# Kernel optimization log

Hardware: AMD Instinct MI355X
Metric: run time of the kernel (lower is better)

## Reference

```python
import jax, jax.numpy as jnp
import numpy as np

B, S, D_IN, D_OUT, HID, E, SHARE, TOPK = 4, 2048, 1024, 1024, 2048, 8, 1, 2


def setup_inputs() -> dict:
    key = jax.random.key(0)
    ks = jax.random.split(key, 12)
    s_in = 1.0 / np.sqrt(D_IN)
    s_hid = 1.0 / np.sqrt(HID)
    return {
        "x": jax.random.normal(ks[0], (B, S, D_IN), jnp.float32),
        "gate_w": jax.random.normal(ks[1], (D_IN, E), jnp.float32) * s_in,
        "gate_b": jnp.zeros((E,), jnp.float32),
        "ew1": jax.random.normal(ks[2], (E, D_IN, HID), jnp.float32) * s_in,
        "eb1": jnp.zeros((E, HID), jnp.float32),
        "ew2": jax.random.normal(ks[3], (E, HID, D_OUT), jnp.float32) * s_hid,
        "eb2": jnp.zeros((E, D_OUT), jnp.float32),
        "sw1": jax.random.normal(ks[4], (SHARE, D_IN, HID), jnp.float32) * s_in,
        "sb1": jnp.zeros((SHARE, HID), jnp.float32),
        "sw2": jax.random.normal(ks[5], (SHARE, HID, D_OUT), jnp.float32) * s_hid,
        "sb2": jnp.zeros((SHARE, D_OUT), jnp.float32),
        "top_k": TOPK,
    }


def reference(x, gate_w, gate_b, ew1, eb1, ew2, eb2, sw1, sb1, sw2, sb2, top_k):
    Bx, Sx, Din = x.shape
    flat_x = x.reshape(-1, Din)                      # [T, D]
    T = flat_x.shape[0]
    Ex = gate_w.shape[1]

    # gate + softmax + top-k, renormalize top-k weights
    logits = flat_x @ gate_w + gate_b                # [T, E]
    expert_weights = jax.nn.softmax(logits, axis=-1)
    topv, topi = jax.lax.top_k(expert_weights, top_k)
    topv = topv / jnp.sum(topv, axis=-1, keepdims=True)

    # per-token combine weights scattered into [T, E] (zero for unselected)
    combine = jnp.zeros((T, Ex), flat_x.dtype)
    combine = combine.at[jnp.arange(T)[:, None], topi].add(topv)

    # expert MLPs (BasicExpert: Linear -> ReLU -> Linear), batched over experts
    h = jax.nn.relu(jnp.einsum("td,edh->teh", flat_x, ew1) + eb1)   # [T, E, H]
    eo = jnp.einsum("teh,eho->teo", h, ew2) + eb2                    # [T, E, O]
    moe_out = jnp.einsum("teo,te->to", eo, combine)                  # [T, O]
    final = moe_out.reshape(Bx, Sx, -1)

    # shared experts added densely to every token
    for k in range(sw1.shape[0]):
        sh = jax.nn.relu(jnp.einsum("bsd,dh->bsh", x, sw1[k]) + sb1[k])
        final = final + jnp.einsum("bsh,ho->bso", sh, sw2[k]) + sb2[k]

    return final, expert_weights
```

## Files before the change

### kernel.cpp

```cpp
#include <hip/hip_runtime.h>
#include <stdint.h>

#define T_TOK 8192
#define DIN   1024
#define DOUT  1024
#define HID   2048
#define NEXP  8
#define MAXN  8192

typedef __attribute__((ext_vector_type(8))) short short8;
typedef __attribute__((ext_vector_type(4))) float floatx4;

__device__ __forceinline__ ushort f2bf(float f) {
    uint32_t u = __float_as_uint(f);
    uint32_t r = (u + 0x7fffu + ((u >> 16) & 1u)) >> 16;
    return (ushort)r;
}

__device__ __forceinline__ void load_lds_16(const ushort* g, ushort* l) {
    __builtin_amdgcn_global_load_lds(
        (const __attribute__((address_space(1))) void*)g,
        (__attribute__((address_space(3))) void*)l, 16, 0, 0);
}

__global__ void convert_x_kernel(const float* __restrict__ in, ushort* __restrict__ out, int n4) {
    int i = blockIdx.x * blockDim.x + threadIdx.x;
    if (i >= n4) return;
    float4 v = ((const float4*)in)[i];
    ushort4 o;
    o.x = f2bf(v.x); o.y = f2bf(v.y); o.z = f2bf(v.z); o.w = f2bf(v.w);
    ((ushort4*)out)[i] = o;
}

__global__ void transpose_bf16_kernel(const float* __restrict__ in, ushort* __restrict__ out,
                                      int R, int C) {
    __shared__ float tile[64][65];
    size_t base = (size_t)blockIdx.z * R * C;
    in  += base;
    out += base;
    int r0 = blockIdx.y * 64, c0 = blockIdx.x * 64;
    int t  = threadIdx.x;
    int rr = t >> 4;
    int cc = (t & 15) * 4;
    for (int p = 0; p < 4; p++) {
        int row = rr + p * 16;
        float4 v = *(const float4*)(in + (size_t)(r0 + row) * C + c0 + cc);
        tile[row][cc + 0] = v.x; tile[row][cc + 1] = v.y;
        tile[row][cc + 2] = v.z; tile[row][cc + 3] = v.w;
    }
    __syncthreads();
    for (int p = 0; p < 4; p++) {
        int orow = rr + p * 16;
        ushort4 o;
        o.x = f2bf(tile[cc + 0][orow]);
        o.y = f2bf(tile[cc + 1][orow]);
        o.z = f2bf(tile[cc + 2][orow]);
        o.w = f2bf(tile[cc + 3][orow]);
        *(ushort4*)(out + (size_t)(c0 + orow) * R + r0 + cc) = o;
    }
}

__global__ void gate_compute_kernel(const float* __restrict__ x, const float* __restrict__ gw,
                                    const float* __restrict__ gb, float* __restrict__ ew_out,
                                    int* __restrict__ te1, int* __restrict__ te2,
                                    float* __restrict__ tw1, float* __restrict__ tw2) {
    int gid  = blockIdx.x * blockDim.x + threadIdx.x;
    int t    = gid >> 6;
    int lane = threadIdx.x & 63;
    if (t >= T_TOK) return;
    float acc[8];
    #pragma unroll
    for (int e = 0; e < 8; e++) acc[e] = 0.f;
    const float* xrow = x + (size_t)t * DIN;
    #pragma unroll
    for (int i = 0; i < 16; i++) {
        int d = lane + i * 64;
        float xv = xrow[d];
        const float4* wr = (const float4*)(gw + (size_t)d * 8);
        float4 w0 = wr[0], w1 = wr[1];
        acc[0] += xv * w0.x; acc[1] += xv * w0.y; acc[2] += xv * w0.z; acc[3] += xv * w0.w;
        acc[4] += xv * w1.x; acc[5] += xv * w1.y; acc[6] += xv * w1.z; acc[7] += xv * w1.w;
    }
    #pragma unroll
    for (int e = 0; e < 8; e++)
        #pragma unroll
        for (int off = 32; off; off >>= 1) acc[e] += __shfl_xor(acc[e], off);
    if (lane == 0) {
        float l[8], mx = -1e30f;
        #pragma unroll
        for (int e = 0; e < 8; e++) { l[e] = acc[e] + gb[e]; mx = fmaxf(mx, l[e]); }
        float s = 0.f;
        #pragma unroll
        for (int e = 0; e < 8; e++) { l[e] = expf(l[e] - mx); s += l[e]; }
        float inv = 1.f / s;
        #pragma unroll
        for (int e = 0; e < 8; e++) { l[e] *= inv; ew_out[(size_t)t * 8 + e] = l[e]; }
        int i1 = 0;
        #pragma unroll
        for (int e = 1; e < 8; e++) if (l[e] > l[i1]) i1 = e;
        int i2 = (i1 == 0) ? 1 : 0;
        #pragma unroll
        for (int e = 0; e < 8; e++) if (e != i1 && l[e] > l[i2]) i2 = e;
        float s2 = l[i1] + l[i2];
        te1[t] = i1; tw1[t] = l[i1] / s2;
        te2[t] = i2; tw2[t] = l[i2] / s2;
    }
}

__global__ void build_lists_kernel(const int* __restrict__ te1, const int* __restrict__ te2,
                                   const float* __restrict__ tw1, const float* __restrict__ tw2,
                                   int* __restrict__ counts, int* __restrict__ etok,
                                   float* __restrict__ ew) {
    __shared__ int lcnt[NEXP];
    __shared__ int gbase[NEXP];
    int tid = threadIdx.x;
    int t = blockIdx.x * 256 + tid;
    if (tid < NEXP) lcnt[tid] = 0;
    __syncthreads();
    int e1 = te1[t], e2 = te2[t];
    float w1 = tw1[t], w2 = tw2[t];
    int r1 = atomicAdd(&lcnt[e1], 1);
    int r2 = atomicAdd(&lcnt[e2], 1);
    __syncthreads();
    if (tid < NEXP) gbase[tid] = atomicAdd(&counts[tid], lcnt[tid]);
    __syncthreads();
    int s1 = gbase[e1] + r1;
    etok[e1 * MAXN + s1] = t;
    ew  [e1 * MAXN + s1] = w1;
    int s2 = gbase[e2] + r2;
    etok[e2 * MAXN + s2] = t;
    ew  [e2 * MAXN + s2] = w2;
}

__global__ void prefix_kernel(const int* __restrict__ counts, int* __restrict__ offsets) {
    if (threadIdx.x == 0 && blockIdx.x == 0) {
        int o = 0;
        for (int e = 0; e < NEXP; e++) { offsets[e] = o; o += counts[e]; }
    }
}


#define STG(slot, j, kh) { \
    load_lds_16(srcA[j] + (size_t)(kh) * 32, dA[j] + (slot) * 8192); \
    load_lds_16(srcB[j] + (size_t)(kh) * 32, dB[j] + (slot) * 8192); }

#define LDA_FRAGS(slot, mh) { \
    const ushort* pa = &lA[(slot) * 8192 + (wave_m * 8 + (mh) * 4) * 512 + lane * 8]; \
    a[0] = *(const short8*)(pa +    0); a[1] = *(const short8*)(pa +  512); \
    a[2] = *(const short8*)(pa + 1024); a[3] = *(const short8*)(pa + 1536); }

#define LDB_FRAGS(slot) { \
    const ushort* pb = &lB[(slot) * 8192 + (wave_n * 4) * 512 + lane * 8]; \
    b[0] = *(const short8*)(pb +    0); b[1] = *(const short8*)(pb +  512); \
    b[2] = *(const short8*)(pb + 1024); b[3] = *(const short8*)(pb + 1536); }

#define MFMA16(mh) { \
    _Pragma("unroll") for (int mt = 0; mt < 4; ++mt) { \
      _Pragma("unroll") for (int nt = 0; nt < 4; ++nt) { \
        acc[(mh)*4+mt][nt] = __builtin_amdgcn_mfma_f32_16x16x32_bf16( \
            a[mt], b[nt], acc[(mh)*4+mt][nt], 0, 0, 0); } } }

#define PH_EVEN(slot, sslot, kh) { \
    LDA_FRAGS(slot, 0); LDB_FRAGS(slot); \
    STG(sslot, 0, kh); \
    __builtin_amdgcn_s_barrier(); \
    asm volatile("s_waitcnt lgkmcnt(0)" ::: "memory"); \
    __builtin_amdgcn_sched_barrier(0); \
    __builtin_amdgcn_s_setprio(1); \
    MFMA16(0); \
    __builtin_amdgcn_s_setprio(0); \
    __builtin_amdgcn_s_barrier(); \
    asm volatile("" ::: "memory"); }

#define PH_ODD(slot, sslot, kh) { \
    LDA_FRAGS(slot, 1); \
    STG(sslot, 1, kh); \
    __builtin_amdgcn_s_barrier(); \
    asm volatile("s_waitcnt lgkmcnt(0)" ::: "memory"); \
    __builtin_amdgcn_sched_barrier(0); \
    __builtin_amdgcn_s_setprio(1); \
    MFMA16(1); \
    __builtin_amdgcn_s_setprio(0); \
    asm volatile("s_waitcnt vmcnt(8)" ::: "memory"); \
    __builtin_amdgcn_s_barrier(); \
    asm volatile("" ::: "memory"); }

template <int MODE>
__global__ __launch_bounds__(512, 2)
void gemm8_kernel(const ushort* __restrict__ Ae, const ushort* __restrict__ Ash,
                  const ushort* __restrict__ Be, const ushort* __restrict__ Bsh,
                  const float* __restrict__ biase, const float* __restrict__ biass,
                  ushort* __restrict__ He, ushort* __restrict__ Hs,
                  float* __restrict__ Out,
                  const int* __restrict__ counts, const int* __restrict__ offsets,
                  const int* __restrict__ expert_tok, const float* __restrict__ expert_w) {
    constexpr int K  = (MODE == 0) ? DIN : HID;
    constexpr int NN = (MODE == 0) ? HID : DOUT;
    constexpr int NH = K / 32;
    constexpr int J  = K / 128;

    const int z  = blockIdx.z;
    const int m0 = blockIdx.y * 256;
    const int n0 = blockIdx.x * 256;

    int cnt = T_TOK, rowbase = 0;
    const ushort* Aptr; const ushort* Bptr; const float* bptr;
    if (z < NEXP) {
        cnt = counts[z];
        if (m0 >= cnt) return;
        rowbase = offsets[z];
        Aptr = Ae; Bptr = Be + (size_t)z * NN * K; bptr = biase + (size_t)z * NN;
    } else {
        Aptr = Ash; Bptr = Bsh; bptr = biass;
    }

    __shared__ ushort lA[4 * 8192];
    __shared__ ushort lB[4 * 8192];
    __shared__ int    rowA[256];
    __shared__ int    rowTok[256];
    __shared__ float  rowW[256];

    const int tid = threadIdx.x;
    if (tid < 256) {
        int g = m0 + tid;
        if (z < NEXP) {
            if constexpr (MODE == 0) {
                rowA[tid] = (g < cnt) ? expert_tok[z * MAXN + g] : 0;
            } else {
                rowA[tid]   = (g < cnt) ? (rowbase + g) : rowbase;
                rowTok[tid] = (g < cnt) ? expert_tok[z * MAXN + g] : 0;
                rowW[tid]   = (g < cnt) ? expert_w[z * MAXN + g] : 0.f;
            }
        } else {
            rowA[tid] = g;
        }
    }
    __syncthreads();

    const int w = tid >> 6, lane = tid & 63;
    const int lm = lane & 15, lq = lane >> 4;
    const int wave_m = w >> 2, wave_n = w & 3;

    const ushort* srcA[2]; const ushort* srcB[2];
    ushort* dA[2]; ushort* dB[2];
    #pragma unroll
    for (int j = 0; j < 2; ++j) {
        int blk = j * 8 + w;
        srcA[j] = Aptr + (size_t)rowA[blk * 16 + lm] * K + lq * 8;
        srcB[j] = Bptr + (size_t)(n0 + blk * 16 + lm) * K + lq * 8;
        dA[j] = &lA[blk * 512];
        dB[j] = &lB[blk * 512];
    }

    floatx4 acc[8][4];
    #pragma unroll
    for (int i = 0; i < 8; ++i)
        #pragma unroll
        for (int jj = 0; jj < 4; ++jj) acc[i][jj] = (floatx4){0.f, 0.f, 0.f, 0.f};

    short8 a[4], b[4];

    STG(0, 0, 0); STG(0, 1, 0);
    STG(1, 0, 1); STG(1, 1, 1);
    STG(2, 0, 2); STG(2, 1, 2);
    asm volatile("s_waitcnt vmcnt(8)" ::: "memory");
    __builtin_amdgcn_s_barrier();
    asm volatile("" ::: "memory");

    for (int j = 0; j < J; ++j) {
        int k4 = 4 * j;
        int kh3 = k4 + 3; if (kh3 > NH - 1) kh3 = NH - 1;
        int kh4 = k4 + 4; if (kh4 > NH - 1) kh4 = NH - 1;
        int kh5 = k4 + 5; if (kh5 > NH - 1) kh5 = NH - 1;
        int kh6 = k4 + 6; if (kh6 > NH - 1) kh6 = NH - 1;
        PH_EVEN(0, 3, kh3);
        PH_ODD (0, 3, kh3);
        PH_EVEN(1, 0, kh4);
        PH_ODD (1, 0, kh4);
        PH_EVEN(2, 1, kh5);
        PH_ODD (2, 1, kh5);
        PH_EVEN(3, 2, kh6);
        PH_ODD (3, 2, kh6);
    }

    asm volatile("s_waitcnt vmcnt(0)" ::: "memory");

    const int wn0 = wave_n * 64;
    #pragma unroll
    for (int mt8 = 0; mt8 < 8; ++mt8) {
        const int rl0 = wave_m * 128 + mt8 * 16 + lq * 4;
        #pragma unroll
        for (int nt = 0; nt < 4; ++nt) {
            const int col = n0 + wn0 + nt * 16 + lm;
            const float bv = bptr[col];
            #pragma unroll
            for (int r = 0; r < 4; ++r) {
                const int rl = rl0 + r;
                const int g  = m0 + rl;
                float v = acc[mt8][nt][r];
                if constexpr (MODE == 0) {
                    v = fmaxf(v + bv, 0.f);
                    if (z < NEXP) {
                        if (g < cnt) He[(size_t)(rowbase + g) * HID + col] = f2bf(v);
                    } else {
                        Hs[(size_t)g * HID + col] = f2bf(v);
                    }
                } else {
                    if (z < NEXP) {
                        if (g < cnt)
                            atomicAdd(&Out[(size_t)rowTok[rl] * DOUT + col], (v + bv) * rowW[rl]);
                    } else {
                        atomicAdd(&Out[(size_t)g * DOUT + col], v + bv);
                    }
                }
            }
        }
    }
}

extern "C" void kernel_launch(void* const* d_in, const int* in_sizes, int n_in,
                              void* d_out, int out_size, void* d_ws, size_t ws_size,
                              hipStream_t stream) {
    const float* x   = (const float*)d_in[0];
    const float* gw  = (const float*)d_in[1];
    const float* gb  = (const float*)d_in[2];
    const float* ew1 = (const float*)d_in[3];
    const float* eb1 = (const float*)d_in[4];
    const float* ew2 = (const float*)d_in[5];
    const float* eb2 = (const float*)d_in[6];
    const float* sw1 = (const float*)d_in[7];
    const float* sb1 = (const float*)d_in[8];
    const float* sw2 = (const float*)d_in[9];
    const float* sb2 = (const float*)d_in[10];

    float* out_final = (float*)d_out;
    float* out_ew    = out_final + (size_t)T_TOK * DOUT;

    char* ws = (char*)d_ws;
    size_t off = 0;
    auto alloc = [&](size_t bytes) -> void* {
        void* p = ws + off;
        off += (bytes + 255) & ~(size_t)255;
        return p;
    };
    ushort* x_bf    = (ushort*)alloc((size_t)T_TOK * DIN * 2);
    ushort* ew1t    = (ushort*)alloc((size_t)NEXP * HID * DIN * 2);
    ushort* ew2t    = (ushort*)alloc((size_t)NEXP * DOUT * HID * 2);
    ushort* sw1t    = (ushort*)alloc((size_t)HID * DIN * 2);
    ushort* sw2t    = (ushort*)alloc((size_t)DOUT * HID * 2);
    ushort* h_buf   = (ushort*)alloc((size_t)T_TOK * 2 * HID * 2);
    ushort* sh_buf  = (ushort*)alloc((size_t)T_TOK * HID * 2);
    int*    counts  = (int*)alloc(NEXP * 4);
    int*    offsets = (int*)alloc(NEXP * 4);
    int*    etok    = (int*)alloc((size_t)NEXP * MAXN * 4);
    float*  ew      = (float*)alloc((size_t)NEXP * MAXN * 4);
    int*    te1     = (int*)alloc((size_t)T_TOK * 4);
    int*    te2     = (int*)alloc((size_t)T_TOK * 4);
    float*  tw1     = (float*)alloc((size_t)T_TOK * 4);
    float*  tw2     = (float*)alloc((size_t)T_TOK * 4);

    hipMemsetAsync(d_out, 0, (size_t)T_TOK * DOUT * 4, stream);
    hipMemsetAsync(counts, 0, NEXP * 4, stream);

    convert_x_kernel<<<(T_TOK * DIN / 4) / 256, 256, 0, stream>>>(x, x_bf, T_TOK * DIN / 4);
    transpose_bf16_kernel<<<dim3(HID / 64, DIN / 64, NEXP), 256, 0, stream>>>(ew1, ew1t, DIN, HID);
    transpose_bf16_kernel<<<dim3(DOUT / 64, HID / 64, NEXP), 256, 0, stream>>>(ew2, ew2t, HID, DOUT);
    transpose_bf16_kernel<<<dim3(HID / 64, DIN / 64, 1), 256, 0, stream>>>(sw1, sw1t, DIN, HID);
    transpose_bf16_kernel<<<dim3(DOUT / 64, HID / 64, 1), 256, 0, stream>>>(sw2, sw2t, HID, DOUT);

    gate_compute_kernel<<<T_TOK / 4, 256, 0, stream>>>(x, gw, gb, out_ew, te1, te2, tw1, tw2);
    build_lists_kernel<<<T_TOK / 256, 256, 0, stream>>>(te1, te2, tw1, tw2, counts, etok, ew);
    prefix_kernel<<<1, 64, 0, stream>>>(counts, offsets);

    gemm8_kernel<0><<<dim3(HID / 256, T_TOK / 256, NEXP + 1), 512, 0, stream>>>(
        x_bf, x_bf, ew1t, sw1t, eb1, sb1, h_buf, sh_buf, nullptr,
        counts, offsets, etok, ew);
    gemm8_kernel<1><<<dim3(DOUT / 256, T_TOK / 256, NEXP + 1), 512, 0, stream>>>(
        h_buf, sh_buf, ew2t, sw2t, eb2, sb2, nullptr, nullptr, out_final,
        counts, offsets, etok, ew);
}
```

Baseline: 694.9 us.

## Use persistent ticket-scheduled GEMMs with compacted tile lists and gathered routed inputs

Both expert GEMMs become persistent kernels with 256 blocks. Each block pulls tiles from a precomputed compact tile list through an atomic ticket, so blocks no longer launch and exit for empty expert tiles. Routed token rows are gathered into a contiguous buffer beforehand, which lets the first GEMM read A with plain strided addresses instead of indirect per-row indices. Smaller changes fold the x-to-bf16 conversion into the gate kernel and merge the shared and expert weight transposes into single launches. In exchange there is an extra gather pass over the routed rows and a serial single-thread tile-list build.

```diff
diff --git a/kernel.cpp b/kernel.cpp
--- a/kernel.cpp
+++ b/kernel.cpp
@@ -7,6 +7,7 @@
 #define HID   2048
 #define NEXP  8
 #define MAXN  8192
+#define NROUTED (2 * T_TOK)
 
 typedef __attribute__((ext_vector_type(8))) short short8;
 typedef __attribute__((ext_vector_type(4))) float floatx4;
@@ -23,21 +24,14 @@
         (__attribute__((address_space(3))) void*)l, 16, 0, 0);
 }
 
-__global__ void convert_x_kernel(const float* __restrict__ in, ushort* __restrict__ out, int n4) {
-    int i = blockIdx.x * blockDim.x + threadIdx.x;
-    if (i >= n4) return;
-    float4 v = ((const float4*)in)[i];
-    ushort4 o;
-    o.x = f2bf(v.x); o.y = f2bf(v.y); o.z = f2bf(v.z); o.w = f2bf(v.w);
-    ((ushort4*)out)[i] = o;
-}
-
-__global__ void transpose_bf16_kernel(const float* __restrict__ in, ushort* __restrict__ out,
+__global__ void transpose_bf16_kernel(const float* __restrict__ in_e, const float* __restrict__ in_s,
+                                      ushort* __restrict__ out_e, ushort* __restrict__ out_s,
                                       int R, int C) {
     __shared__ float tile[64][65];
-    size_t base = (size_t)blockIdx.z * R * C;
-    in  += base;
-    out += base;
+    const float* in; ushort* out;
+    int zz = blockIdx.z;
+    if (zz < NEXP) { in = in_e + (size_t)zz * R * C; out = out_e + (size_t)zz * R * C; }
+    else           { in = in_s;                      out = out_s; }
     int r0 = blockIdx.y * 64, c0 = blockIdx.x * 64;
     int t  = threadIdx.x;
     int rr = t >> 4;
@@ -63,7 +57,8 @@
 __global__ void gate_compute_kernel(const float* __restrict__ x, const float* __restrict__ gw,
                                     const float* __restrict__ gb, float* __restrict__ ew_out,
                                     int* __restrict__ te1, int* __restrict__ te2,
-                                    float* __restrict__ tw1, float* __restrict__ tw2) {
+                                    float* __restrict__ tw1, float* __restrict__ tw2,
+                                    ushort* __restrict__ xb) {
     int gid  = blockIdx.x * blockDim.x + threadIdx.x;
     int t    = gid >> 6;
     int lane = threadIdx.x & 63;
@@ -72,10 +67,12 @@
     #pragma unroll
     for (int e = 0; e < 8; e++) acc[e] = 0.f;
     const float* xrow = x + (size_t)t * DIN;
+    ushort* xbrow = xb + (size_t)t * DIN;
     #pragma unroll
     for (int i = 0; i < 16; i++) {
         int d = lane + i * 64;
         float xv = xrow[d];
+        xbrow[d] = f2bf(xv);
         const float4* wr = (const float4*)(gw + (size_t)d * 8);
         float4 w0 = wr[0], w1 = wr[1];
         acc[0] += xv * w0.x; acc[1] += xv * w0.y; acc[2] += xv * w0.z; acc[3] += xv * w0.w;
@@ -132,11 +129,44 @@
     ew  [e2 * MAXN + s2] = w2;
 }
 
-__global__ void prefix_kernel(const int* __restrict__ counts, int* __restrict__ offsets) {
+__global__ void prefix_tiles_kernel(const int* __restrict__ counts, int* __restrict__ offsets,
+                                    int* __restrict__ tiles1, int* __restrict__ tiles2,
+                                    int* __restrict__ meta) {
     if (threadIdx.x == 0 && blockIdx.x == 0) {
-        int o = 0;
-        for (int e = 0; e < NEXP; e++) { offsets[e] = o; o += counts[e]; }
-    }
+        int o = 0, ny[9];
+        for (int e = 0; e < NEXP; e++) {
+            offsets[e] = o; o += counts[e];
+            ny[e] = (counts[e] + 255) >> 8;
+        }
+        offsets[8] = o;
+        ny[8] = T_TOK / 256;
+        int i1 = 0, i2 = 0;
+        for (int zi = 0; zi < 9; zi++) {
+            int z = (zi == 0) ? 8 : zi - 1;
+            for (int xx = 0; xx < HID / 256; xx++)
+                for (int yy = 0; yy < ny[z]; yy++)
+                    tiles1[i1++] = (z << 10) | (yy << 4) | xx;
+        }
+        for (int zi = 0; zi < 9; zi++) {
+            int z = (zi == 0) ? 8 : zi - 1;
+            for (int xx = 0; xx < DOUT / 256; xx++)
+                for (int yy = 0; yy < ny[z]; yy++)
+                    tiles2[i2++] = (z << 10) | (yy << 4) | xx;
+        }
+        meta[0] = i1; meta[1] = i2;
+    }
+}
+
+__global__ void gather_xg_kernel(const ushort* __restrict__ x_bf, ushort* __restrict__ xg,
+                                 const int* __restrict__ offsets, const int* __restrict__ etok) {
+    int p = blockIdx.x;
+    int e = 0;
+    #pragma unroll
+    for (int i = 1; i < NEXP; i++) if (p >= offsets[i]) e = i;
+    int tok = etok[e * MAXN + (p - offsets[e])];
+    const ushort4* src = (const ushort4*)(x_bf + (size_t)tok * DIN);
+    ushort4*       dst = (ushort4*)(xg + (size_t)p * DIN);
+    dst[threadIdx.x] = src[threadIdx.x];
 }
 
 
@@ -187,130 +217,135 @@
 
 template <int MODE>
 __global__ __launch_bounds__(512, 2)
-void gemm8_kernel(const ushort* __restrict__ Ae, const ushort* __restrict__ Ash,
-                  const ushort* __restrict__ Be, const ushort* __restrict__ Bsh,
+void gemm_persist(const ushort* __restrict__ Ar, const ushort* __restrict__ As,
+                  const ushort* __restrict__ Be, const ushort* __restrict__ Bs,
                   const float* __restrict__ biase, const float* __restrict__ biass,
                   ushort* __restrict__ He, ushort* __restrict__ Hs,
                   float* __restrict__ Out,
                   const int* __restrict__ counts, const int* __restrict__ offsets,
-                  const int* __restrict__ expert_tok, const float* __restrict__ expert_w) {
-    constexpr int K  = (MODE == 0) ? DIN : HID;
-    constexpr int NN = (MODE == 0) ? HID : DOUT;
-    constexpr int NH = K / 32;
-    constexpr int J  = K / 128;
-
-    const int z  = blockIdx.z;
-    const int m0 = blockIdx.y * 256;
-    const int n0 = blockIdx.x * 256;
-
-    int cnt = T_TOK, rowbase = 0;
-    const ushort* Aptr; const ushort* Bptr; const float* bptr;
-    if (z < NEXP) {
-        cnt = counts[z];
-        if (m0 >= cnt) return;
-        rowbase = offsets[z];
-        Aptr = Ae; Bptr = Be + (size_t)z * NN * K; bptr = biase + (size_t)z * NN;
-    } else {
-        Aptr = Ash; Bptr = Bsh; bptr = biass;
-    }
+                  const int* __restrict__ etok, const float* __restrict__ ew,
+                  const int* __restrict__ tiles, const int* __restrict__ meta,
+                  int* __restrict__ ticket) {
+    constexpr int K   = (MODE == 0) ? DIN : HID;
+    constexpr int NN  = (MODE == 0) ? HID : DOUT;
+    constexpr int NHc = K / 32;
+    constexpr int J   = K / 128;
 
     __shared__ ushort lA[4 * 8192];
     __shared__ ushort lB[4 * 8192];
-    __shared__ int    rowA[256];
     __shared__ int    rowTok[256];
     __shared__ float  rowW[256];
-
-    const int tid = threadIdx.x;
-    if (tid < 256) {
-        int g = m0 + tid;
-        if (z < NEXP) {
-            if constexpr (MODE == 0) {
-                rowA[tid] = (g < cnt) ? expert_tok[z * MAXN + g] : 0;
-            } else {
-                rowA[tid]   = (g < cnt) ? (rowbase + g) : rowbase;
-                rowTok[tid] = (g < cnt) ? expert_tok[z * MAXN + g] : 0;
-                rowW[tid]   = (g < cnt) ? expert_w[z * MAXN + g] : 0.f;
-            }
-        } else {
-            rowA[tid] = g;
-        }
-    }
-    __syncthreads();
-
+    __shared__ int    sh_t;
+
+    const int tid  = threadIdx.x;
+    const int ntiles = meta[MODE];
     const int w = tid >> 6, lane = tid & 63;
     const int lm = lane & 15, lq = lane >> 4;
     const int wave_m = w >> 2, wave_n = w & 3;
 
-    const ushort* srcA[2]; const ushort* srcB[2];
-    ushort* dA[2]; ushort* dB[2];
-    #pragma unroll
-    for (int j = 0; j < 2; ++j) {
-        int blk = j * 8 + w;
-        srcA[j] = Aptr + (size_t)rowA[blk * 16 + lm] * K + lq * 8;
-        srcB[j] = Bptr + (size_t)(n0 + blk * 16 + lm) * K + lq * 8;
-        dA[j] = &lA[blk * 512];
-        dB[j] = &lB[blk * 512];
-    }
-
-    floatx4 acc[8][4];
-    #pragma unroll
-    for (int i = 0; i < 8; ++i)
-        #pragma unroll
-        for (int jj = 0; jj < 4; ++jj) acc[i][jj] = (floatx4){0.f, 0.f, 0.f, 0.f};
-
-    short8 a[4], b[4];
-
-    STG(0, 0, 0); STG(0, 1, 0);
-    STG(1, 0, 1); STG(1, 1, 1);
-    STG(2, 0, 2); STG(2, 1, 2);
-    asm volatile("s_waitcnt vmcnt(8)" ::: "memory");
-    __builtin_amdgcn_s_barrier();
-    asm volatile("" ::: "memory");
-
-    for (int j = 0; j < J; ++j) {
-        int k4 = 4 * j;
-        int kh3 = k4 + 3; if (kh3 > NH - 1) kh3 = NH - 1;
-        int kh4 = k4 + 4; if (kh4 > NH - 1) kh4 = NH - 1;
-        int kh5 = k4 + 5; if (kh5 > NH - 1) kh5 = NH - 1;
-        int kh6 = k4 + 6; if (kh6 > NH - 1) kh6 = NH - 1;
-        PH_EVEN(0, 3, kh3);
-        PH_ODD (0, 3, kh3);
-        PH_EVEN(1, 0, kh4);
-        PH_ODD (1, 0, kh4);
-        PH_EVEN(2, 1, kh5);
-        PH_ODD (2, 1, kh5);
-        PH_EVEN(3, 2, kh6);
-        PH_ODD (3, 2, kh6);
-    }
-
-    asm volatile("s_waitcnt vmcnt(0)" ::: "memory");
-
-    const int wn0 = wave_n * 64;
-    #pragma unroll
-    for (int mt8 = 0; mt8 < 8; ++mt8) {
-        const int rl0 = wave_m * 128 + mt8 * 16 + lq * 4;
-        #pragma unroll
-        for (int nt = 0; nt < 4; ++nt) {
-            const int col = n0 + wn0 + nt * 16 + lm;
-            const float bv = bptr[col];
+    for (;;) {
+        if (tid == 0) sh_t = atomicAdd(ticket, 1);
+        __syncthreads();
+        const int t = sh_t;
+        if (t >= ntiles) return;
+
+        const int tx = tiles[t];
+        const int x  = tx & 15;
+        const int y  = (tx >> 4) & 63;
+        const int z  = (tx >> 10) & 15;
+        const int m0 = y * 256, n0 = x * 256;
+
+        int cnt, rowbase;
+        const ushort* Aptr; const ushort* Bptr; const float* bptr;
+        if (z < NEXP) {
+            cnt = counts[z]; rowbase = offsets[z];
+            Aptr = Ar; Bptr = Be + (size_t)z * NN * K; bptr = biase + (size_t)z * NN;
+        } else {
+            cnt = T_TOK; rowbase = 0;
+            Aptr = As; Bptr = Bs; bptr = biass;
+        }
+        const int arow0 = rowbase + m0;
+
+        if constexpr (MODE == 1) {
+            if (tid < 256 && z < NEXP) {
+                int g = m0 + tid;
+                rowTok[tid] = (g < cnt) ? etok[z * MAXN + g] : 0;
+                rowW[tid]   = (g < cnt) ? ew[z * MAXN + g] : 0.f;
+            }
+        }
+        __syncthreads();
+
+        const ushort* srcA[2]; const ushort* srcB[2];
+        ushort* dA[2]; ushort* dB[2];
+        #pragma unroll
+        for (int j = 0; j < 2; ++j) {
+            int blk = j * 8 + w;
+            srcA[j] = Aptr + (size_t)(arow0 + blk * 16 + lm) * K + lq * 8;
+            srcB[j] = Bptr + (size_t)(n0 + blk * 16 + lm) * K + lq * 8;
+            dA[j] = &lA[blk * 512];
+            dB[j] = &lB[blk * 512];
+        }
+
+        floatx4 acc[8][4];
+        #pragma unroll
+        for (int i = 0; i < 8; ++i)
             #pragma unroll
-            for (int r = 0; r < 4; ++r) {
-                const int rl = rl0 + r;
-                const int g  = m0 + rl;
-                float v = acc[mt8][nt][r];
-                if constexpr (MODE == 0) {
-                    v = fmaxf(v + bv, 0.f);
-                    if (z < NEXP) {
-                        if (g < cnt) He[(size_t)(rowbase + g) * HID + col] = f2bf(v);
+            for (int jj = 0; jj < 4; ++jj) acc[i][jj] = (floatx4){0.f, 0.f, 0.f, 0.f};
+
+        short8 a[4], b[4];
+
+        STG(0, 0, 0); STG(0, 1, 0);
+        STG(1, 0, 1); STG(1, 1, 1);
+        STG(2, 0, 2); STG(2, 1, 2);
+        asm volatile("s_waitcnt vmcnt(8)" ::: "memory");
+        __builtin_amdgcn_s_barrier();
+        asm volatile("" ::: "memory");
+
+        for (int j = 0; j < J; ++j) {
+            int k4 = 4 * j;
+            int kh3 = k4 + 3; if (kh3 > NHc - 1) kh3 = NHc - 1;
+            int kh4 = k4 + 4; if (kh4 > NHc - 1) kh4 = NHc - 1;
+            int kh5 = k4 + 5; if (kh5 > NHc - 1) kh5 = NHc - 1;
+            int kh6 = k4 + 6; if (kh6 > NHc - 1) kh6 = NHc - 1;
+            PH_EVEN(0, 3, kh3);
+            PH_ODD (0, 3, kh3);
+            PH_EVEN(1, 0, kh4);
+            PH_ODD (1, 0, kh4);
+            PH_EVEN(2, 1, kh5);
+            PH_ODD (2, 1, kh5);
+            PH_EVEN(3, 2, kh6);
+            PH_ODD (3, 2, kh6);
+        }
+
+        asm volatile("s_waitcnt vmcnt(0)" ::: "memory");
+
+        const int wn0 = wave_n * 64;
+        #pragma unroll
+        for (int mt8 = 0; mt8 < 8; ++mt8) {
+            const int rl0 = wave_m * 128 + mt8 * 16 + lq * 4;
+            #pragma unroll
+            for (int nt = 0; nt < 4; ++nt) {
+                const int col = n0 + wn0 + nt * 16 + lm;
+                const float bv = bptr[col];
+                #pragma unroll
+                for (int r = 0; r < 4; ++r) {
+                    const int rl = rl0 + r;
+                    const int g  = m0 + rl;
+                    float v = acc[mt8][nt][r];
+                    if constexpr (MODE == 0) {
+                        v = fmaxf(v + bv, 0.f);
+                        if (z < NEXP) {
+                            if (g < cnt) He[(size_t)(rowbase + g) * HID + col] = f2bf(v);
+                        } else {
+                            Hs[(size_t)g * HID + col] = f2bf(v);
+                        }
                     } else {
-                        Hs[(size_t)g * HID + col] = f2bf(v);
-                    }
-                } else {
-                    if (z < NEXP) {
-                        if (g < cnt)
-                            atomicAdd(&Out[(size_t)rowTok[rl] * DOUT + col], (v + bv) * rowW[rl]);
-                    } else {
-                        atomicAdd(&Out[(size_t)g * DOUT + col], v + bv);
+                        if (z < NEXP) {
+                            if (g < cnt)
+                                atomicAdd(&Out[(size_t)rowTok[rl] * DOUT + col], (v + bv) * rowW[rl]);
+                        } else {
+                            atomicAdd(&Out[(size_t)g * DOUT + col], v + bv);
+                        }
                     }
                 }
             }
@@ -344,14 +379,21 @@
         return p;
     };
     ushort* x_bf    = (ushort*)alloc((size_t)T_TOK * DIN * 2);
+    ushort* xg      = (ushort*)alloc((size_t)(NROUTED + 256) * DIN * 2);
     ushort* ew1t    = (ushort*)alloc((size_t)NEXP * HID * DIN * 2);
     ushort* ew2t    = (ushort*)alloc((size_t)NEXP * DOUT * HID * 2);
     ushort* sw1t    = (ushort*)alloc((size_t)HID * DIN * 2);
     ushort* sw2t    = (ushort*)alloc((size_t)DOUT * HID * 2);
-    ushort* h_buf   = (ushort*)alloc((size_t)T_TOK * 2 * HID * 2);
-    ushort* sh_buf  = (ushort*)alloc((size_t)T_TOK * HID * 2);
-    int*    counts  = (int*)alloc(NEXP * 4);
-    int*    offsets = (int*)alloc(NEXP * 4);
+    ushort* h_buf   = (ushort*)alloc((size_t)(NROUTED + T_TOK) * HID * 2);
+    ushort* sh_buf  = h_buf + (size_t)NROUTED * HID;
+    int*    ctrl    = (int*)alloc(16 * 4);
+    int*    counts  = ctrl;
+    int*    ticket1 = ctrl + 8;
+    int*    ticket2 = ctrl + 9;
+    int*    offsets = (int*)alloc(16 * 4);
+    int*    tiles1  = (int*)alloc(2048 * 4);
+    int*    tiles2  = (int*)alloc(2048 * 4);
+    int*    meta    = (int*)alloc(256);
     int*    etok    = (int*)alloc((size_t)NEXP * MAXN * 4);
     float*  ew      = (float*)alloc((size_t)NEXP * MAXN * 4);
     int*    te1     = (int*)alloc((size_t)T_TOK * 4);
@@ -360,22 +402,22 @@
     float*  tw2     = (float*)alloc((size_t)T_TOK * 4);
 
     hipMemsetAsync(d_out, 0, (size_t)T_TOK * DOUT * 4, stream);
-    hipMemsetAsync(counts, 0, NEXP * 4, stream);
-
-    convert_x_kernel<<<(T_TOK * DIN / 4) / 256, 256, 0, stream>>>(x, x_bf, T_TOK * DIN / 4);
-    transpose_bf16_kernel<<<dim3(HID / 64, DIN / 64, NEXP), 256, 0, stream>>>(ew1, ew1t, DIN, HID);
-    transpose_bf16_kernel<<<dim3(DOUT / 64, HID / 64, NEXP), 256, 0, stream>>>(ew2, ew2t, HID, DOUT);
-    transpose_bf16_kernel<<<dim3(HID / 64, DIN / 64, 1), 256, 0, stream>>>(sw1, sw1t, DIN, HID);
-    transpose_bf16_kernel<<<dim3(DOUT / 64, HID / 64, 1), 256, 0, stream>>>(sw2, sw2t, HID, DOUT);
-
-    gate_compute_kernel<<<T_TOK / 4, 256, 0, stream>>>(x, gw, gb, out_ew, te1, te2, tw1, tw2);
+    hipMemsetAsync(ctrl, 0, 16 * 4, stream);
+
+    transpose_bf16_kernel<<<dim3(HID / 64, DIN / 64, NEXP + 1), 256, 0, stream>>>(
+        ew1, sw1, ew1t, sw1t, DIN, HID);
+    transpose_bf16_kernel<<<dim3(DOUT / 64, HID / 64, NEXP + 1), 256, 0, stream>>>(
+        ew2, sw2, ew2t, sw2t, HID, DOUT);
+
+    gate_compute_kernel<<<T_TOK / 4, 256, 0, stream>>>(x, gw, gb, out_ew, te1, te2, tw1, tw2, x_bf);
     build_lists_kernel<<<T_TOK / 256, 256, 0, stream>>>(te1, te2, tw1, tw2, counts, etok, ew);
-    prefix_kernel<<<1, 64, 0, stream>>>(counts, offsets);
-
-    gemm8_kernel<0><<<dim3(HID / 256, T_TOK / 256, NEXP + 1), 512, 0, stream>>>(
-        x_bf, x_bf, ew1t, sw1t, eb1, sb1, h_buf, sh_buf, nullptr,
-        counts, offsets, etok, ew);
-    gemm8_kernel<1><<<dim3(DOUT / 256, T_TOK / 256, NEXP + 1), 512, 0, stream>>>(
+    prefix_tiles_kernel<<<1, 64, 0, stream>>>(counts, offsets, tiles1, tiles2, meta);
+    gather_xg_kernel<<<NROUTED, 256, 0, stream>>>(x_bf, xg, offsets, etok);
+
+    gemm_persist<0><<<256, 512, 0, stream>>>(
+        xg, x_bf, ew1t, sw1t, eb1, sb1, h_buf, sh_buf, nullptr,
+        counts, offsets, etok, ew, tiles1, meta, ticket1);
+    gemm_persist<1><<<256, 512, 0, stream>>>(
         h_buf, sh_buf, ew2t, sw2t, eb2, sb2, nullptr, nullptr, out_final,
-        counts, offsets, etok, ew);
-}
+        counts, offsets, etok, ew, tiles2, meta, ticket2);
+}
```

New measurement: 776.1 us. 1.12x slower.

## Switch GEMM to two-stage LDS pipeline and fuse x conversion into gate

Applied to the files above, without the earlier changes.

Replaces the four-stage LDS ring in the grouped GEMM with a double-buffered loop and raises the occupancy hint to four blocks per CU, cutting shared memory use. The x fp32-to-bf16 conversion is folded into the gating kernel, and expert and shared weight transposes are merged into single launches. The goal is higher occupancy and fewer launches. The cost is a full vmem wait each K step, which reduces load/compute overlap, and possible register pressure or spills under the tighter launch bound.

```diff
diff --git a/kernel.cpp b/kernel.cpp
--- a/kernel.cpp
+++ b/kernel.cpp
@@ -23,21 +23,14 @@
         (__attribute__((address_space(3))) void*)l, 16, 0, 0);
 }
 
-__global__ void convert_x_kernel(const float* __restrict__ in, ushort* __restrict__ out, int n4) {
-    int i = blockIdx.x * blockDim.x + threadIdx.x;
-    if (i >= n4) return;
-    float4 v = ((const float4*)in)[i];
-    ushort4 o;
-    o.x = f2bf(v.x); o.y = f2bf(v.y); o.z = f2bf(v.z); o.w = f2bf(v.w);
-    ((ushort4*)out)[i] = o;
-}
-
-__global__ void transpose_bf16_kernel(const float* __restrict__ in, ushort* __restrict__ out,
+__global__ void transpose_bf16_kernel(const float* __restrict__ in_e, const float* __restrict__ in_s,
+                                      ushort* __restrict__ out_e, ushort* __restrict__ out_s,
                                       int R, int C) {
     __shared__ float tile[64][65];
-    size_t base = (size_t)blockIdx.z * R * C;
-    in  += base;
-    out += base;
+    const float* in; ushort* out;
+    int zz = blockIdx.z;
+    if (zz < NEXP) { in = in_e + (size_t)zz * R * C; out = out_e + (size_t)zz * R * C; }
+    else           { in = in_s;                      out = out_s; }
     int r0 = blockIdx.y * 64, c0 = blockIdx.x * 64;
     int t  = threadIdx.x;
     int rr = t >> 4;
@@ -63,7 +56,8 @@
 __global__ void gate_compute_kernel(const float* __restrict__ x, const float* __restrict__ gw,
                                     const float* __restrict__ gb, float* __restrict__ ew_out,
                                     int* __restrict__ te1, int* __restrict__ te2,
-                                    float* __restrict__ tw1, float* __restrict__ tw2) {
+                                    float* __restrict__ tw1, float* __restrict__ tw2,
+                                    ushort* __restrict__ xb) {
     int gid  = blockIdx.x * blockDim.x + threadIdx.x;
     int t    = gid >> 6;
     int lane = threadIdx.x & 63;
@@ -72,10 +66,12 @@
     #pragma unroll
     for (int e = 0; e < 8; e++) acc[e] = 0.f;
     const float* xrow = x + (size_t)t * DIN;
+    ushort* xbrow = xb + (size_t)t * DIN;
     #pragma unroll
     for (int i = 0; i < 16; i++) {
         int d = lane + i * 64;
         float xv = xrow[d];
+        xbrow[d] = f2bf(xv);
         const float4* wr = (const float4*)(gw + (size_t)d * 8);
         float4 w0 = wr[0], w1 = wr[1];
         acc[0] += xv * w0.x; acc[1] += xv * w0.y; acc[2] += xv * w0.z; acc[3] += xv * w0.w;
@@ -160,44 +156,18 @@
         acc[(mh)*4+mt][nt] = __builtin_amdgcn_mfma_f32_16x16x32_bf16( \
             a[mt], b[nt], acc[(mh)*4+mt][nt], 0, 0, 0); } } }
 
-#define PH_EVEN(slot, sslot, kh) { \
-    LDA_FRAGS(slot, 0); LDB_FRAGS(slot); \
-    STG(sslot, 0, kh); \
-    __builtin_amdgcn_s_barrier(); \
-    asm volatile("s_waitcnt lgkmcnt(0)" ::: "memory"); \
-    __builtin_amdgcn_sched_barrier(0); \
-    __builtin_amdgcn_s_setprio(1); \
-    MFMA16(0); \
-    __builtin_amdgcn_s_setprio(0); \
-    __builtin_amdgcn_s_barrier(); \
-    asm volatile("" ::: "memory"); }
-
-#define PH_ODD(slot, sslot, kh) { \
-    LDA_FRAGS(slot, 1); \
-    STG(sslot, 1, kh); \
-    __builtin_amdgcn_s_barrier(); \
-    asm volatile("s_waitcnt lgkmcnt(0)" ::: "memory"); \
-    __builtin_amdgcn_sched_barrier(0); \
-    __builtin_amdgcn_s_setprio(1); \
-    MFMA16(1); \
-    __builtin_amdgcn_s_setprio(0); \
-    asm volatile("s_waitcnt vmcnt(8)" ::: "memory"); \
-    __builtin_amdgcn_s_barrier(); \
-    asm volatile("" ::: "memory"); }
-
 template <int MODE>
-__global__ __launch_bounds__(512, 2)
-void gemm8_kernel(const ushort* __restrict__ Ae, const ushort* __restrict__ Ash,
-                  const ushort* __restrict__ Be, const ushort* __restrict__ Bsh,
-                  const float* __restrict__ biase, const float* __restrict__ biass,
-                  ushort* __restrict__ He, ushort* __restrict__ Hs,
-                  float* __restrict__ Out,
-                  const int* __restrict__ counts, const int* __restrict__ offsets,
-                  const int* __restrict__ expert_tok, const float* __restrict__ expert_w) {
+__global__ __launch_bounds__(512, 4)
+void gemm2s_kernel(const ushort* __restrict__ Ae, const ushort* __restrict__ Ash,
+                   const ushort* __restrict__ Be, const ushort* __restrict__ Bsh,
+                   const float* __restrict__ biase, const float* __restrict__ biass,
+                   ushort* __restrict__ He, ushort* __restrict__ Hs,
+                   float* __restrict__ Out,
+                   const int* __restrict__ counts, const int* __restrict__ offsets,
+                   const int* __restrict__ expert_tok, const float* __restrict__ expert_w) {
     constexpr int K  = (MODE == 0) ? DIN : HID;
     constexpr int NN = (MODE == 0) ? HID : DOUT;
     constexpr int NH = K / 32;
-    constexpr int J  = K / 128;
 
     const int z  = blockIdx.z;
     const int m0 = blockIdx.y * 256;
@@ -214,8 +184,8 @@
         Aptr = Ash; Bptr = Bsh; bptr = biass;
     }
 
-    __shared__ ushort lA[4 * 8192];
-    __shared__ ushort lB[4 * 8192];
+    __shared__ ushort lA[2 * 8192];
+    __shared__ ushort lB[2 * 8192];
     __shared__ int    rowA[256];
     __shared__ int    rowTok[256];
     __shared__ float  rowW[256];
@@ -261,29 +231,32 @@
     short8 a[4], b[4];
 
     STG(0, 0, 0); STG(0, 1, 0);
-    STG(1, 0, 1); STG(1, 1, 1);
-    STG(2, 0, 2); STG(2, 1, 2);
-    asm volatile("s_waitcnt vmcnt(8)" ::: "memory");
+    asm volatile("s_waitcnt vmcnt(0)" ::: "memory");
     __builtin_amdgcn_s_barrier();
     asm volatile("" ::: "memory");
 
-    for (int j = 0; j < J; ++j) {
-        int k4 = 4 * j;
-        int kh3 = k4 + 3; if (kh3 > NH - 1) kh3 = NH - 1;
-        int kh4 = k4 + 4; if (kh4 > NH - 1) kh4 = NH - 1;
-        int kh5 = k4 + 5; if (kh5 > NH - 1) kh5 = NH - 1;
-        int kh6 = k4 + 6; if (kh6 > NH - 1) kh6 = NH - 1;
-        PH_EVEN(0, 3, kh3);
-        PH_ODD (0, 3, kh3);
-        PH_EVEN(1, 0, kh4);
-        PH_ODD (1, 0, kh4);
-        PH_EVEN(2, 1, kh5);
-        PH_ODD (2, 1, kh5);
-        PH_EVEN(3, 2, kh6);
-        PH_ODD (3, 2, kh6);
-    }
-
-    asm volatile("s_waitcnt vmcnt(0)" ::: "memory");
+    for (int p = 0; p < NH; ++p) {
+        const int s  = p & 1;
+        const int ns = s ^ 1;
+        const int np = (p + 1 < NH) ? (p + 1) : (NH - 1);
+        STG(ns, 0, np);
+        LDA_FRAGS(s, 0); LDB_FRAGS(s);
+        asm volatile("s_waitcnt lgkmcnt(0)" ::: "memory");
+        __builtin_amdgcn_sched_barrier(0);
+        __builtin_amdgcn_s_setprio(1);
+        MFMA16(0);
+        __builtin_amdgcn_s_setprio(0);
+        STG(ns, 1, np);
+        LDA_FRAGS(s, 1);
+        asm volatile("s_waitcnt lgkmcnt(0)" ::: "memory");
+        __builtin_amdgcn_sched_barrier(0);
+        __builtin_amdgcn_s_setprio(1);
+        MFMA16(1);
+        __builtin_amdgcn_s_setprio(0);
+        asm volatile("s_waitcnt vmcnt(0)" ::: "memory");
+        __builtin_amdgcn_s_barrier();
+        asm volatile("" ::: "memory");
+    }
 
     const int wn0 = wave_n * 64;
     #pragma unroll
@@ -362,20 +335,19 @@
     hipMemsetAsync(d_out, 0, (size_t)T_TOK * DOUT * 4, stream);
     hipMemsetAsync(counts, 0, NEXP * 4, stream);
 
-    convert_x_kernel<<<(T_TOK * DIN / 4) / 256, 256, 0, stream>>>(x, x_bf, T_TOK * DIN / 4);
-    transpose_bf16_kernel<<<dim3(HID / 64, DIN / 64, NEXP), 256, 0, stream>>>(ew1, ew1t, DIN, HID);
-    transpose_bf16_kernel<<<dim3(DOUT / 64, HID / 64, NEXP), 256, 0, stream>>>(ew2, ew2t, HID, DOUT);
-    transpose_bf16_kernel<<<dim3(HID / 64, DIN / 64, 1), 256, 0, stream>>>(sw1, sw1t, DIN, HID);
-    transpose_bf16_kernel<<<dim3(DOUT / 64, HID / 64, 1), 256, 0, stream>>>(sw2, sw2t, HID, DOUT);
-
-    gate_compute_kernel<<<T_TOK / 4, 256, 0, stream>>>(x, gw, gb, out_ew, te1, te2, tw1, tw2);
+    transpose_bf16_kernel<<<dim3(HID / 64, DIN / 64, NEXP + 1), 256, 0, stream>>>(
+        ew1, sw1, ew1t, sw1t, DIN, HID);
+    transpose_bf16_kernel<<<dim3(DOUT / 64, HID / 64, NEXP + 1), 256, 0, stream>>>(
+        ew2, sw2, ew2t, sw2t, HID, DOUT);
+
+    gate_compute_kernel<<<T_TOK / 4, 256, 0, stream>>>(x, gw, gb, out_ew, te1, te2, tw1, tw2, x_bf);
     build_lists_kernel<<<T_TOK / 256, 256, 0, stream>>>(te1, te2, tw1, tw2, counts, etok, ew);
     prefix_kernel<<<1, 64, 0, stream>>>(counts, offsets);
 
-    gemm8_kernel<0><<<dim3(HID / 256, T_TOK / 256, NEXP + 1), 512, 0, stream>>>(
+    gemm2s_kernel<0><<<dim3(HID / 256, T_TOK / 256, NEXP + 1), 512, 0, stream>>>(
         x_bf, x_bf, ew1t, sw1t, eb1, sb1, h_buf, sh_buf, nullptr,
         counts, offsets, etok, ew);
-    gemm8_kernel<1><<<dim3(DOUT / 256, T_TOK / 256, NEXP + 1), 512, 0, stream>>>(
+    gemm2s_kernel<1><<<dim3(DOUT / 256, T_TOK / 256, NEXP + 1), 512, 0, stream>>>(
         h_buf, sh_buf, ew2t, sw2t, eb2, sb2, nullptr, nullptr, out_final,
         counts, offsets, etok, ew);
 }
```

New measurement: 1.967 ms. +183.1%, slower.
